# Optimization experiments

Measured on AMD Instinct MI355X. Metric: run time of the kernel, lower is better.

The kernel has to match this reference:

```python
import jax, jax.numpy as jnp
import numpy as np

# PDEEval config (init_kwargs)
MIN_VALUE = 0.0
MAX_VALUE = 1.0
MIN_CONC = 0.0
# concrete diffusion PDE config
DT = 0.2          # explicit-Euler step size
T_STEPS = 16      # == fill_max of t, >= int(t.max()); extra steps are exact no-ops (clip is idempotent)

B, C, H, W = 32, 1, 512, 512


def _laplacian(c):
    # 5-point periodic stencil on the [B, C, H, W] field
    return (jnp.roll(c, 1, axis=2) + jnp.roll(c, -1, axis=2)
            + jnp.roll(c, 1, axis=3) + jnp.roll(c, -1, axis=3)
            - 4.0 * c)


def setup_inputs() -> dict:
    key = jax.random.key(0)
    k1, k2, k3 = jax.random.split(key, 3)
    x = jax.random.uniform(k1, (B, C, H, W), dtype=jnp.float32)  # concentrations in [0, 1]
    t = jax.random.randint(k2, (B,), 0, T_STEPS)                 # per-sample number of PDE steps
    d_coef = jax.random.uniform(k3, (1,), dtype=jnp.float32)     # learned diffusivity scale (params provider)
    return {"x": x, "t": t, "d_coef": d_coef}


def reference(x, t, d_coef):
    def step(y, i):
        mask = (t > i)[:, None, None, None]                       # [B,1,1,1] which samples still evolve
        conc = jnp.where(y > MIN_CONC, y, 0.0)                    # concentration = y * (y > min_concentration)
        # params provider: per-sample diffusivity from mean concentration
        D = d_coef[0] * jax.nn.sigmoid(conc.mean(axis=(1, 2, 3)))  # [B]
        diff = D[:, None, None, None] * DT * _laplacian(conc)
        y = jnp.where(mask, y + diff, y)                          # scatter-add back only to masked samples
        return jnp.clip(y, MIN_VALUE, MAX_VALUE), None

    y, _ = jax.lax.scan(step, x, jnp.arange(T_STEPS))
    return y
```

## Files before the change

kernel.cpp:

```cpp
#include <hip/hip_runtime.h>
#include <math.h>

#define BB 32
#define HH 512
#define WW 512
#define T_STEPS 16
#define DT_C 0.2f
#define HW (HH * WW)
#define RBLK 16

#define NF 8
#define TS 64
#define ITR 86
#define ITC 80
#define PADC 84


__device__ __forceinline__ float block_sum_256(float v) {
    __shared__ float lds[4];
#pragma unroll
    for (int off = 32; off > 0; off >>= 1)
        v += __shfl_down(v, off, 64);
    const int lane = threadIdx.x & 63;
    const int wid  = threadIdx.x >> 6;
    if (lane == 0) lds[wid] = v;
    __syncthreads();
    float s = 0.f;
    if (threadIdx.x == 0) s = lds[0] + lds[1] + lds[2] + lds[3];
    return s;
}

__global__ __launch_bounds__(256) void reduce_x_kernel(
        const float* __restrict__ x, const int* __restrict__ t,
        float* __restrict__ partials) {
    const int b = blockIdx.y;
    if (t[b] <= 0) return;
    const float4* xb = (const float4*)(x + (size_t)b * HW);
    float v = 0.f;
    const int base = blockIdx.x * (HW / 4 / RBLK);
#pragma unroll
    for (int k = 0; k < 16; k++) {
        float4 c = xb[base + k * 256 + threadIdx.x];
        v += (c.x + c.y) + (c.z + c.w);
    }
    float s = block_sum_256(v);
    if (threadIdx.x == 0) partials[b * RBLK + blockIdx.x] = s;
}

__global__ __launch_bounds__(256) void fused_kernel(
        const float* __restrict__ src,
        float* __restrict__ adst,
        float* __restrict__ fdst,
        const float* __restrict__ x,
        float* __restrict__ out,
        const int* __restrict__ t,
        const float* __restrict__ partials,
        const float* __restrict__ dcoef,
        int base) {
    const int b = blockIdx.y;
    const int tb = t[b];
    const int tx = blockIdx.x & 7;
    const int ty = blockIdx.x >> 3;
    const int h0 = ty * TS;
    const int w0 = tx * TS;

    if (tb <= base) {
        if (base == 0 && tb == 0) {
            const float4* s4 = (const float4*)(x + (size_t)b * HW);
            float4* d4 = (float4*)(out + (size_t)b * HW);
            for (int j = threadIdx.x; j < TS * (TS / 4); j += 256) {
                const int r = j >> 4, c4 = j & 15;
                const int idx = (h0 + r) * (WW / 4) + (w0 >> 2) + c4;
                float4 v = s4[idx];
                v.x = fminf(fmaxf(v.x, 0.f), 1.f);
                v.y = fminf(fmaxf(v.y, 0.f), 1.f);
                v.z = fminf(fmaxf(v.z, 0.f), 1.f);
                v.w = fminf(fmaxf(v.w, 0.f), 1.f);
                d4[idx] = v;
            }
        }
        return;
    }

    int nst = tb - base;
    if (nst > NF) nst = NF;
    float* dstp = (tb <= base + NF) ? fdst : adst;

    float psum = 0.f;
#pragma unroll
    for (int k = 0; k < RBLK; k++) psum += partials[b * RBLK + k];
    const float f = dcoef[0] * (1.0f / (1.0f + expf(-psum * (1.0f / (float)HW)))) * DT_C;

    __shared__ __align__(16) float buf[ITR][PADC];

    const float* sb = src + (size_t)b * HW;
    for (int j = threadIdx.x; j < ITR * (ITC / 4); j += 256) {
        const int r  = j / (ITC / 4);
        const int cg = j - r * (ITC / 4);
        const int gr  = (h0 - 11 + r) & (HH - 1);
        const int gc4 = ((w0 >> 2) - 2 + cg) & (WW / 4 - 1);
        *(float4*)(&buf[r][cg * 4]) = *(const float4*)(sb + gr * WW + gc4 * 4);
    }
    __syncthreads();

    const int ln  = threadIdx.x & 63;
    const int siw = ln / 20;
    const int g   = ln - siw * 20;
    const int s   = (threadIdx.x >> 6) * 3 + siw;
    const bool act = (siw < 3);
    const int r1 = 1 + 7 * s;
    const int cb = 4 * g;

    float4 cur[7];
    if (act) {
#pragma unroll
        for (int j = 0; j < 7; j++)
            cur[j] = *(const float4*)(&buf[r1 + j][cb]);
    }

    for (int it = 0; it < nst; it++) {
        if (act) {
            float4 up = *(const float4*)(&buf[r1 - 1][cb]);
            const float4 h8v = *(const float4*)(&buf[r1 + 7][cb]);
#pragma unroll
            for (int j = 0; j < 7; j++) {
                const float4 c = cur[j];
                const float4 d = (j == 6) ? h8v : cur[j + 1];
                const float L = __shfl_up(c.w, 1, 64);
                const float R = __shfl_down(c.x, 1, 64);
                float4 o;
                o.x = fmaf(f, L   + c.y + up.x + d.x - 4.f * c.x, c.x);
                o.y = fmaf(f, c.x + c.z + up.y + d.y - 4.f * c.y, c.y);
                o.z = fmaf(f, c.y + c.w + up.z + d.z - 4.f * c.z, c.z);
                o.w = fmaf(f, c.z + R   + up.w + d.w - 4.f * c.w, c.w);
                o.x = fminf(fmaxf(o.x, 0.f), 1.f);
                o.y = fminf(fmaxf(o.y, 0.f), 1.f);
                o.z = fminf(fmaxf(o.z, 0.f), 1.f);
                o.w = fminf(fmaxf(o.w, 0.f), 1.f);
                cur[j] = o;
                up = c;
            }
        }
        __syncthreads();
        if (act) {
            *(float4*)(&buf[r1][cb])     = cur[0];
            *(float4*)(&buf[r1 + 6][cb]) = cur[6];
        }
        __syncthreads();
    }

    if (act && g >= 2 && g < 18) {
        float* db = dstp + (size_t)b * HW;
        const int gcol = w0 - 8 + cb;
#pragma unroll
        for (int j = 0; j < 7; j++) {
            const int lr = r1 + j;
            if (lr >= 11 && lr < 75)
                *(float4*)(db + (size_t)(h0 + lr - 11) * WW + gcol) = cur[j];
        }
    }
}

extern "C" void kernel_launch(void* const* d_in, const int* in_sizes, int n_in,
                              void* d_out, int out_size, void* d_ws, size_t ws_size,
                              hipStream_t stream) {
    const float* x     = (const float*)d_in[0];
    const int*   t     = (const int*)d_in[1];
    const float* dcoef = (const float*)d_in[2];
    float* out = (float*)d_out;

    float* partials = (float*)d_ws;
    float* f1       = (float*)((char*)d_ws + 4096);

    reduce_x_kernel<<<dim3(RBLK, BB), dim3(256), 0, stream>>>(x, t, partials);

    fused_kernel<<<dim3(64, BB), dim3(256), 0, stream>>>(x,  f1, out, x, out, t, partials, dcoef, 0);
    fused_kernel<<<dim3(64, BB), dim3(256), 0, stream>>>(f1, f1, out, x, out, t, partials, dcoef, 8);
}
```

Measured before the change: 56.34 us.

## Use taller 128x64 tiles with 8-wide strips and halo-only shared memory

```diff
diff --git a/kernel.cpp b/kernel.cpp
--- a/kernel.cpp
+++ b/kernel.cpp
@@ -10,10 +10,12 @@
 #define RBLK 16
 
 #define NF 8
-#define TS 64
-#define ITR 86
+#define TSC 64
+#define TSR 128
+#define ITR 146
 #define ITC 80
-#define PADC 84
+#define NSLOT 50
+#define SLOTW 84
 
 
 __device__ __forceinline__ float block_sum_256(float v) {
@@ -45,6 +47,14 @@
     }
     float s = block_sum_256(v);
     if (threadIdx.x == 0) partials[b * RBLK + blockIdx.x] = s;
+}
+
+__device__ __forceinline__ float4 clamp4(float4 v) {
+    v.x = fminf(fmaxf(v.x, 0.f), 1.f);
+    v.y = fminf(fmaxf(v.y, 0.f), 1.f);
+    v.z = fminf(fmaxf(v.z, 0.f), 1.f);
+    v.w = fminf(fmaxf(v.w, 0.f), 1.f);
+    return v;
 }
 
 __global__ __launch_bounds__(256) void fused_kernel(
@@ -61,22 +71,17 @@
     const int tb = t[b];
     const int tx = blockIdx.x & 7;
     const int ty = blockIdx.x >> 3;
-    const int h0 = ty * TS;
-    const int w0 = tx * TS;
+    const int h0 = ty * TSR;
+    const int w0 = tx * TSC;
 
     if (tb <= base) {
         if (base == 0 && tb == 0) {
             const float4* s4 = (const float4*)(x + (size_t)b * HW);
             float4* d4 = (float4*)(out + (size_t)b * HW);
-            for (int j = threadIdx.x; j < TS * (TS / 4); j += 256) {
+            for (int j = threadIdx.x; j < TSR * (TSC / 4); j += 256) {
                 const int r = j >> 4, c4 = j & 15;
                 const int idx = (h0 + r) * (WW / 4) + (w0 >> 2) + c4;
-                float4 v = s4[idx];
-                v.x = fminf(fmaxf(v.x, 0.f), 1.f);
-                v.y = fminf(fmaxf(v.y, 0.f), 1.f);
-                v.z = fminf(fmaxf(v.z, 0.f), 1.f);
-                v.w = fminf(fmaxf(v.w, 0.f), 1.f);
-                d4[idx] = v;
+                d4[idx] = clamp4(s4[idx]);
             }
         }
         return;
@@ -91,72 +96,91 @@
     for (int k = 0; k < RBLK; k++) psum += partials[b * RBLK + k];
     const float f = dcoef[0] * (1.0f / (1.0f + expf(-psum * (1.0f / (float)HW)))) * DT_C;
 
-    __shared__ __align__(16) float buf[ITR][PADC];
+    __shared__ __align__(16) float pub[NSLOT][SLOTW];
+
+    const int ln  = threadIdx.x & 63;
+    const int si  = ln / 10;
+    const int g   = ln - si * 10;
+    const bool act = (si < 6);
+    const int s   = act ? ((threadIdx.x >> 6) * 6 + si) : 0;
+    const int r1  = 1 + 6 * s;
+    const int cb  = 8 * (act ? g : 0);
 
     const float* sb = src + (size_t)b * HW;
-    for (int j = threadIdx.x; j < ITR * (ITC / 4); j += 256) {
-        const int r  = j / (ITC / 4);
-        const int cg = j - r * (ITC / 4);
-        const int gr  = (h0 - 11 + r) & (HH - 1);
+    const int gc = (w0 - 8 + cb) & (WW - 1);
+
+    float4 cA[6], cB[6];
+#pragma unroll
+    for (int j = 0; j < 6; j++) {
+        const int gr = (h0 - 9 + r1 + j) & (HH - 1);
+        cA[j] = *(const float4*)(sb + gr * WW + gc);
+        cB[j] = *(const float4*)(sb + gr * WW + gc + 4);
+    }
+    if (threadIdx.x < 40) {
+        const int r  = threadIdx.x / 20;
+        const int cg = threadIdx.x % 20;
+        const int lr = r ? (ITR - 1) : 0;
+        const int gr = (h0 - 9 + lr) & (HH - 1);
         const int gc4 = ((w0 >> 2) - 2 + cg) & (WW / 4 - 1);
-        *(float4*)(&buf[r][cg * 4]) = *(const float4*)(sb + gr * WW + gc4 * 4);
+        *(float4*)(&pub[r ? (NSLOT - 1) : 0][cg * 4]) =
+            *(const float4*)(sb + gr * WW + gc4 * 4);
+    }
+    if (act) {
+        *(float4*)(&pub[2 * s + 1][cb])     = cA[0];
+        *(float4*)(&pub[2 * s + 1][cb + 4]) = cB[0];
+        *(float4*)(&pub[2 * s + 2][cb])     = cA[5];
+        *(float4*)(&pub[2 * s + 2][cb + 4]) = cB[5];
     }
     __syncthreads();
 
-    const int ln  = threadIdx.x & 63;
-    const int siw = ln / 20;
-    const int g   = ln - siw * 20;
-    const int s   = (threadIdx.x >> 6) * 3 + siw;
-    const bool act = (siw < 3);
-    const int r1 = 1 + 7 * s;
-    const int cb = 4 * g;
-
-    float4 cur[7];
-    if (act) {
-#pragma unroll
-        for (int j = 0; j < 7; j++)
-            cur[j] = *(const float4*)(&buf[r1 + j][cb]);
-    }
-
     for (int it = 0; it < nst; it++) {
-        if (act) {
-            float4 up = *(const float4*)(&buf[r1 - 1][cb]);
-            const float4 h8v = *(const float4*)(&buf[r1 + 7][cb]);
-#pragma unroll
-            for (int j = 0; j < 7; j++) {
-                const float4 c = cur[j];
-                const float4 d = (j == 6) ? h8v : cur[j + 1];
-                const float L = __shfl_up(c.w, 1, 64);
-                const float R = __shfl_down(c.x, 1, 64);
-                float4 o;
-                o.x = fmaf(f, L   + c.y + up.x + d.x - 4.f * c.x, c.x);
-                o.y = fmaf(f, c.x + c.z + up.y + d.y - 4.f * c.y, c.y);
-                o.z = fmaf(f, c.y + c.w + up.z + d.z - 4.f * c.z, c.z);
-                o.w = fmaf(f, c.z + R   + up.w + d.w - 4.f * c.w, c.w);
-                o.x = fminf(fmaxf(o.x, 0.f), 1.f);
-                o.y = fminf(fmaxf(o.y, 0.f), 1.f);
-                o.z = fminf(fmaxf(o.z, 0.f), 1.f);
-                o.w = fminf(fmaxf(o.w, 0.f), 1.f);
-                cur[j] = o;
-                up = c;
-            }
+        float4 uA = *(const float4*)(&pub[2 * s][cb]);
+        float4 uB = *(const float4*)(&pub[2 * s][cb + 4]);
+        const float4 dA = *(const float4*)(&pub[2 * s + 3][cb]);
+        const float4 dB = *(const float4*)(&pub[2 * s + 3][cb + 4]);
+#pragma unroll
+        for (int j = 0; j < 6; j++) {
+            const float4 a = cA[j];
+            const float4 q = cB[j];
+            const float4 nA = (j == 5) ? dA : cA[j + 1];
+            const float4 nB = (j == 5) ? dB : cB[j + 1];
+            const float L = __shfl_up(q.w, 1, 64);
+            const float R = __shfl_down(a.x, 1, 64);
+            float4 oA, oB;
+            oA.x = fmaf(f, L   + a.y + uA.x + nA.x - 4.f * a.x, a.x);
+            oA.y = fmaf(f, a.x + a.z + uA.y + nA.y - 4.f * a.y, a.y);
+            oA.z = fmaf(f, a.y + a.w + uA.z + nA.z - 4.f * a.z, a.z);
+            oA.w = fmaf(f, a.z + q.x + uA.w + nA.w - 4.f * a.w, a.w);
+            oB.x = fmaf(f, a.w + q.y + uB.x + nB.x - 4.f * q.x, q.x);
+            oB.y = fmaf(f, q.x + q.z + uB.y + nB.y - 4.f * q.y, q.y);
+            oB.z = fmaf(f, q.y + q.w + uB.z + nB.z - 4.f * q.z, q.z);
+            oB.w = fmaf(f, q.z + R   + uB.w + nB.w - 4.f * q.w, q.w);
+            cA[j] = clamp4(oA);
+            cB[j] = clamp4(oB);
+            uA = a;
+            uB = q;
         }
         __syncthreads();
         if (act) {
-            *(float4*)(&buf[r1][cb])     = cur[0];
-            *(float4*)(&buf[r1 + 6][cb]) = cur[6];
+            *(float4*)(&pub[2 * s + 1][cb])     = cA[0];
+            *(float4*)(&pub[2 * s + 1][cb + 4]) = cB[0];
+            *(float4*)(&pub[2 * s + 2][cb])     = cA[5];
+            *(float4*)(&pub[2 * s + 2][cb + 4]) = cB[5];
         }
         __syncthreads();
     }
 
-    if (act && g >= 2 && g < 18) {
+    if (act && g >= 1 && g < 9) {
         float* db = dstp + (size_t)b * HW;
         const int gcol = w0 - 8 + cb;
 #pragma unroll
-        for (int j = 0; j < 7; j++) {
+        for (int j = 0; j < 6; j++) {
             const int lr = r1 + j;
-            if (lr >= 11 && lr < 75)
-                *(float4*)(db + (size_t)(h0 + lr - 11) * WW + gcol) = cur[j];
+            if (lr >= 9 && lr < 137) {
+                float* p = db + (size_t)(h0 + lr - 9) * WW + gcol;
+                *(float4*)p       = cA[j];
+                *(float4*)(p + 4) = cB[j];
+            }
         }
     }
 }
@@ -174,6 +198,6 @@
 
     reduce_x_kernel<<<dim3(RBLK, BB), dim3(256), 0, stream>>>(x, t, partials);
 
-    fused_kernel<<<dim3(64, BB), dim3(256), 0, stream>>>(x,  f1, out, x, out, t, partials, dcoef, 0);
-    fused_kernel<<<dim3(64, BB), dim3(256), 0, stream>>>(f1, f1, out, x, out, t, partials, dcoef, 8);
-}
+    fused_kernel<<<dim3(32, BB), dim3(256), 0, stream>>>(x,  f1, out, x, out, t, partials, dcoef, 0);
+    fused_kernel<<<dim3(32, BB), dim3(256), 0, stream>>>(f1, f1, out, x, out, t, partials, dcoef, 8);
+}
```

Result: faster. 52.73 us, median of 2 (-6.4%).
